# Kernel optimization log

Hardware: AMD Instinct MI355X
Metric: run time of the kernel (lower is better)

Reference implementation:

```python
import jax, jax.numpy as jnp
import numpy as np

T, B, H = 512, 256, 512


def setup_inputs() -> dict:
    key = jax.random.key(0)
    k1, k2, k3, k4, k5 = jax.random.split(key, 5)
    scale_i = 1.0 / np.sqrt(H)
    return {
        "h0": jax.random.normal(k1, (B, H), dtype=jnp.float32),
        "ins": jax.random.normal(k2, (T, B, H), dtype=jnp.float32),
        "Wi": jax.random.normal(k3, (H, 3 * H), dtype=jnp.float32) * scale_i,
        "bi": jnp.zeros((3 * H,), dtype=jnp.float32),
        "Wh": jax.random.normal(k4, (H, 3 * H), dtype=jnp.float32) * scale_i,
        "bhn": jnp.zeros((H,), dtype=jnp.float32),
        "resets": jax.random.randint(k5, (T, B), 0, 2).astype(jnp.bool_),
    }


def reference(h0, ins, Wi, bi, Wh, bhn, resets):
    # flax GRUCell math: r = sig(x Wir + bir + h Whr); z = sig(x Wiz + biz + h Whz)
    def step(h, xr):
        x, reset = xr                       # x: [B,H], reset: [B]
        h = jnp.where(reset[:, None], jnp.zeros_like(h), h)  # reset carry to zeros
        gi = x @ Wi + bi                    # [B,3H]
        gh = h @ Wh                         # [B,3H]
        ir, iz, inn = jnp.split(gi, 3, axis=-1)
        hr, hz, hn = jnp.split(gh, 3, axis=-1)
        r = jax.nn.sigmoid(ir + hr)
        z = jax.nn.sigmoid(iz + hz)
        n = jnp.tanh(inn + r * (hn + bhn))
        h_new = (1.0 - z) * n + z * h
        return h_new, h_new

    _, ys = jax.lax.scan(step, h0, (ins, resets))
    return ys                               # [T,B,H]
```

## Files before the change

kernel.cpp:

```cpp
#include <hip/hip_runtime.h>

#define T_ 512
#define B_ 256
#define H_ 512
#define NBINS 4112
typedef __bf16 bf16_t;
typedef __bf16 bf16x8 __attribute__((ext_vector_type(8)));
typedef float f32x4 __attribute__((ext_vector_type(4)));

__device__ __forceinline__ float bf2f(unsigned short u) {
  unsigned x = ((unsigned)u) << 16; float f; __builtin_memcpy(&f, &x, 4); return f;
}
__device__ __forceinline__ bf16x8 pack2(f32x4 a, f32x4 b) {
  bf16x8 w;
#pragma unroll
  for (int i = 0; i < 4; ++i) { w[i] = (bf16_t)a[i]; w[i + 4] = (bf16_t)b[i]; }
  return w;
}
__device__ __forceinline__ void st_sc1(float* p, float v) {
  asm volatile("global_store_dword %0, %1, off sc0 sc1" :: "v"(p), "v"(v) : "memory");
}
__device__ __forceinline__ void ld8_sc1(const float* p0, const float* p1,
                                        const float* p2, const float* p3,
                                        const float* p4, const float* p5,
                                        const float* p6, const float* p7,
                                        f32x4& v0, f32x4& v1, f32x4& v2, f32x4& v3,
                                        f32x4& v4, f32x4& v5, f32x4& v6, f32x4& v7) {
  asm volatile(
      "global_load_dwordx4 %0, %8, off sc0 sc1\n\t"
      "global_load_dwordx4 %1, %9, off sc0 sc1\n\t"
      "global_load_dwordx4 %2, %10, off sc0 sc1\n\t"
      "global_load_dwordx4 %3, %11, off sc0 sc1\n\t"
      "global_load_dwordx4 %4, %12, off sc0 sc1\n\t"
      "global_load_dwordx4 %5, %13, off sc0 sc1\n\t"
      "global_load_dwordx4 %6, %14, off sc0 sc1\n\t"
      "global_load_dwordx4 %7, %15, off sc0 sc1\n\t"
      "s_waitcnt vmcnt(0)"
      : "=&v"(v0), "=&v"(v1), "=&v"(v2), "=&v"(v3),
        "=&v"(v4), "=&v"(v5), "=&v"(v6), "=&v"(v7)
      : "v"(p0), "v"(p1), "v"(p2), "v"(p3), "v"(p4), "v"(p5), "v"(p6), "v"(p7)
      : "memory");
}
__device__ __forceinline__ float sigm(float x) { return 1.f / (1.f + __expf(-x)); }
__device__ __forceinline__ float tanh_(float a) { return 1.f - 2.f / (__expf(2.f * a) + 1.f); }

__global__ __launch_bounds__(64) void zero_meta(int* __restrict__ flags,
                                                int* __restrict__ bar) {
  int i = threadIdx.x;
  if (i < 4) flags[i] = 0;
  if (i < 8) bar[i] = 0;
}

__global__ __launch_bounds__(256) void detect_resets(const void* __restrict__ rst,
                                                     int n, int* __restrict__ flags) {
  const int* pi = (const int*)rst;
  const float* pf = (const float*)rst;
  int a = 0, bq = 0, c = 0;
  int nq = n >> 2;
  for (int i = blockIdx.x * 256 + threadIdx.x; i < nq; i += gridDim.x * 256) {
    int v = pi[i];
    if (v != 0 && v != 1) a = 1;
    float f = pf[i];
    if (!(f == 0.0f || f == 1.0f)) bq = 1;
    if ((i & 1) && v != 0) c = 1;
  }
  if (a) atomicOr(&flags[0], 1);
  if (bq) atomicOr(&flags[1], 1);
  if (c) atomicOr(&flags[2], 1);
}

__global__ __launch_bounds__(256) void convert_resets(const void* __restrict__ rst,
                                                      const int* __restrict__ flags,
                                                      unsigned char* __restrict__ r8,
                                                      int n) {
  const int* pi = (const int*)rst;
  const float* pf = (const float*)rst;
  int mode;
  if (flags[0] == 0) mode = flags[2] ? 0 : 3;
  else if (flags[1] == 0) mode = 1;
  else mode = 2;
  for (int i = blockIdx.x * 256 + threadIdx.x; i < n; i += gridDim.x * 256) {
    unsigned char v;
    if (mode == 0)      v = (unsigned char)(pi[i] != 0);
    else if (mode == 3) v = (unsigned char)(pi[2 * i] != 0);
    else if (mode == 1) v = (unsigned char)(pf[i] != 0.0f);
    else                v = ((const unsigned char*)rst)[i] ? 1 : 0;
    r8[i] = v;
  }
}

__global__ __launch_bounds__(256) void build_wc(const float* __restrict__ Wi,
                                                const float* __restrict__ Wh,
                                                bf16_t* __restrict__ Wc) {
  int id = blockIdx.x * 256 + threadIdx.x;
  int koct = id / 1536, n = id % 1536;
  const float* src = (koct < 64) ? Wi : Wh;
  int kk = (koct & 63) * 8;
  bf16x8 w;
#pragma unroll
  for (int e = 0; e < 8; ++e) w[e] = (bf16_t)src[(size_t)(kk + e) * 1536 + n];
  *(bf16x8*)(Wc + (size_t)id * 8) = w;
}

__device__ __forceinline__ int bucket_of(int t, int rs, int& p) {
  p = (t == 0 || rs) ? 0 : p + 1;
  return (p > 0) ? (p + 1) : ((t == 0 && !rs) ? 1 : 0);
}

__global__ __launch_bounds__(1024) void bins_kernel(const unsigned char* __restrict__ r8,
                                                    int* __restrict__ cur,
                                                    unsigned int* __restrict__ elem) {
  extern __shared__ int sm[];
  int* s0 = sm;
  int* s1 = sm + 8192;
  const int tid = threadIdx.x;
  for (int i = tid; i < 8192; i += 1024) s0[i] = 0;
  __syncthreads();
  if (tid < 256) {
    int b = tid, sub = b >> 5, p = 0;
    for (int t = 0; t < T_; ++t) {
      int bk = bucket_of(t, r8[t * B_ + b], p);
      atomicAdd(&s0[bk * 8 + sub], 1);
    }
  }
  __syncthreads();
  int* a = s0;
  int* bb = s1;
  for (int d = 1; d < 8192; d <<= 1) {
    for (int i = tid; i < 8192; i += 1024) bb[i] = a[i] + ((i >= d) ? a[i - d] : 0);
    __syncthreads();
    int* t = a; a = bb; bb = t;
  }
  for (int i = tid; i <= NBINS; i += 1024) cur[i] = (i == 0) ? 0 : a[i - 1];
  for (int i = tid; i < 8192; i += 1024)
    bb[i] = (i == 0) ? 0 : ((i <= NBINS) ? a[i - 1] : 0);
  __syncthreads();
  if (tid < 256) {
    int b = tid, sub = b >> 5, p = 0;
    for (int t = 0; t < T_; ++t) {
      int bk = bucket_of(t, r8[t * B_ + b], p);
      int pos = atomicAdd(&bb[bk * 8 + sub], 1);
      elem[pos] = (unsigned)(t * B_ + b);
    }
  }
}

template <int NRGC, int LDB>
__device__ __forceinline__ void mm3(const char* lds, const char* W, int q,
                                    int rgb, int span, int nrgd, int am, int aq,
                                    f32x4 (&acc)[3][NRGC]) {
  const char* Bp = W + (size_t)(q * 16 + am) * 16;
#pragma unroll
  for (int ks = 0; ks < 16; ++ks) {
    const int koct = ks * 4 + aq;
    const char* bb = Bp + (size_t)koct * 24576;
    bf16x8 b0 = *(const bf16x8*)(bb);
    bf16x8 b1 = *(const bf16x8*)(bb + 8192);
    bf16x8 b2 = *(const bf16x8*)(bb + 16384);
#pragma unroll
    for (int rg = 0; rg < NRGC; ++rg) {
      if (rg >= rgb && rg < rgb + span && rg < nrgd) {
        const int ar = rg * 16 + am;
        bf16x8 af = *(const bf16x8*)(lds + (size_t)ar * LDB +
                                     ((koct * 16) ^ ((ar & 7) << 4)));
        acc[0][rg] = __builtin_amdgcn_mfma_f32_16x16x32_bf16(af, b0, acc[0][rg], 0, 0, 0);
        acc[1][rg] = __builtin_amdgcn_mfma_f32_16x16x32_bf16(af, b1, acc[1][rg], 0, 0, 0);
        acc[2][rg] = __builtin_amdgcn_mfma_f32_16x16x32_bf16(af, b2, acc[2][rg], 0, 0, 0);
      }
    }
  }
}

template <int NKS, int NRGC, int LDB>
__device__ __forceinline__ void mm_block(const char* lds, const char* W, int q,
                                         int rgb, int span, int nrgd, int am, int aq,
                                         f32x4 (&acc)[4][NRGC]) {
  const char* Bp = W + (size_t)(q * 16 + am) * 16;
#pragma unroll
  for (int ks = 0; ks < NKS; ++ks) {
    const int koct = ks * 4 + aq;
    const char* bb = Bp + (size_t)koct * 24576;
    bf16x8 b0 = *(const bf16x8*)(bb);
    bf16x8 b1 = *(const bf16x8*)(bb + 8192);
    bf16x8 b2 = *(const bf16x8*)(bb + 16384);
#pragma unroll
    for (int rg = 0; rg < NRGC; ++rg) {
      if (rg >= rgb && rg < rgb + span && rg < nrgd) {
        const int ar = rg * 16 + am;
        bf16x8 af = *(const bf16x8*)(lds + (size_t)ar * LDB +
                                     ((koct * 16) ^ ((ar & 7) << 4)));
        acc[0][rg] = __builtin_amdgcn_mfma_f32_16x16x32_bf16(af, b0, acc[0][rg], 0, 0, 0);
        acc[1][rg] = __builtin_amdgcn_mfma_f32_16x16x32_bf16(af, b1, acc[1][rg], 0, 0, 0);
        if (ks < 16)
          acc[2][rg] = __builtin_amdgcn_mfma_f32_16x16x32_bf16(af, b2, acc[2][rg], 0, 0, 0);
        else
          acc[3][rg] = __builtin_amdgcn_mfma_f32_16x16x32_bf16(af, b2, acc[3][rg], 0, 0, 0);
      }
    }
  }
}

__global__ __launch_bounds__(512) void xonly_gemm(
    const float* __restrict__ ins, const bf16_t* __restrict__ Wic,
    const float* __restrict__ bi, const float* __restrict__ bhn,
    const unsigned char* __restrict__ r8, float* __restrict__ out) {
  extern __shared__ char lds[];
  const int u = blockIdx.x;
  const int tid = threadIdx.x, lane = tid & 63, w = tid >> 6;
  const int am = lane & 15, aq = lane >> 4;
  {
    const int tr = tid >> 2, tl = tid & 3;
    const float* xs = ins + ((size_t)u * 128 + tr) * 512;
    const int swz = (tr & 7) << 4;
    char* lrp = lds + tr * 1024;
#pragma unroll 4
    for (int s2 = 0; s2 < 16; ++s2) {
      const int ko = tl + 4 * s2;
      f32x4 a0 = __builtin_nontemporal_load((const f32x4*)(xs + ko * 8));
      f32x4 a1 = __builtin_nontemporal_load((const f32x4*)(xs + ko * 8 + 4));
      *(bf16x8*)(lrp + ((ko * 16) ^ swz)) = pack2(a0, a1);
    }
  }
  __syncthreads();
#pragma unroll 1
  for (int s = 0; s < 4; ++s) {
    const int q = w + 8 * s;
    f32x4 acc[3][8];
#pragma unroll
    for (int gg = 0; gg < 3; ++gg)
#pragma unroll
      for (int r = 0; r < 8; ++r) acc[gg][r] = (f32x4){0.f, 0.f, 0.f, 0.f};
    mm3<8, 1024>(lds, (const char*)Wic, q, 0, 8, 8, am, aq, acc);
    const int j = q * 16 + am;
    const float bir = bi[j], biz = bi[512 + j], bin = bi[1024 + j], bh = bhn[j];
#pragma unroll
    for (int rg = 0; rg < 8; ++rg) {
#pragma unroll
      for (int qq = 0; qq < 4; ++qq) {
        const int e = u * 128 + rg * 16 + aq * 4 + qq;
        if (r8[e]) {
          float r = sigm(acc[0][rg][qq] + bir);
          float z = sigm(acc[1][rg][qq] + biz);
          float n = tanh_(acc[2][rg][qq] + bin + r * bh);
          float v = (1.f - z) * n;
          float* op = out + (size_t)e * 512 + j;
          if (e >= (T_ - 1) * B_ || r8[e + B_]) __builtin_nontemporal_store(v, op);
          else st_sc1(op, v);
        }
      }
    }
  }
}

__global__ __launch_bounds__(512) void gru_pool(
    const float* __restrict__ ins, const float* __restrict__ h0,
    const bf16_t* __restrict__ Wc, const float* __restrict__ bi,
    const float* __restrict__ bhn, const unsigned char* __restrict__ r8,
    const unsigned int* __restrict__ elem, const int* __restrict__ cur,
    int* __restrict__ bar, float* __restrict__ out) {
  extern __shared__ char lds[];
  const int tid = threadIdx.x, lane = tid & 63, w = tid >> 6;
  const int am = lane & 15, aq = lane >> 4;
  const int nbg = gridDim.x, bg = blockIdx.x;
  int done = 0;

  for (int it = 1; it <= 513; ++it) {
    const int beg = cur[it * 8];
    const int cnt = cur[(it + 1) * 8] - beg;
    if (it >= 2 && cnt == 0) break;
    if (cnt > 0) {
      const int ntiles = (cnt + 63) >> 6;
      int lg = 0;
      while (lg < 4 && (ntiles << lg) < nbg) ++lg;
      const int nitems = ntiles << lg;
      const int Q = 32 >> lg;
      for (int i = bg; i < nitems; i += nbg) {
        const int u = i >> lg, jc = i & ((1 << lg) - 1);
        __syncthreads();
        {
          const int tr = tid >> 3, tl = tid & 7;
          const int row = u * 64 + tr;
          const float* xs = nullptr;
          const float* ph = nullptr;
          if (row < cnt) {
            const unsigned e = elem[beg + row];
            xs = ins + (size_t)e * 512;
            ph = (e < 256) ? (h0 + (size_t)e * 512) : (out + ((size_t)e - 256) * 512);
          }
          const int swz = (tr & 7) << 4;
          char* lrp = lds + tr * 2048;
#pragma unroll
          for (int s2 = 0; s2 < 8; ++s2) {
            const int ko = tl + 8 * s2;
            bf16x8 wv;
            if (xs) {
              f32x4 a0 = __builtin_nontemporal_load((const f32x4*)(xs + ko * 8));
              f32x4 a1 = __builtin_nontemporal_load((const f32x4*)(xs + ko * 8 + 4));
              wv = pack2(a0, a1);
            } else {
#pragma unroll
              for (int z = 0; z < 8; ++z) wv[z] = (bf16_t)0.f;
            }
            *(bf16x8*)(lrp + ((ko * 16) ^ swz)) = wv;
          }
          if (ph) {
#pragma unroll 1
            for (int hb = 0; hb < 2; ++hb) {
              f32x4 hv[8];
              const float* hp[8];
#pragma unroll
              for (int s2 = 0; s2 < 4; ++s2) {
                const int ko = tl + 8 * (8 + hb * 4 + s2);
                hp[2 * s2] = ph + (ko & 63) * 8;
                hp[2 * s2 + 1] = ph + (ko & 63) * 8 + 4;
              }
              ld8_sc1(hp[0], hp[1], hp[2], hp[3], hp[4], hp[5], hp[6], hp[7],
                      hv[0], hv[1], hv[2], hv[3], hv[4], hv[5], hv[6], hv[7]);
#pragma unroll
              for (int s2 = 0; s2 < 4; ++s2) {
                const int ko = tl + 8 * (8 + hb * 4 + s2);
                *(bf16x8*)(lrp + ((ko * 16) ^ swz)) = pack2(hv[2 * s2], hv[2 * s2 + 1]);
              }
            }
          } else {
#pragma unroll
            for (int s2 = 0; s2 < 8; ++s2) {
              const int ko = tl + 8 * (8 + s2);
              bf16x8 wv;
#pragma unroll
              for (int z = 0; z < 8; ++z) wv[z] = (bf16_t)0.f;
              *(bf16x8*)(lrp + ((ko * 16) ^ swz)) = wv;
            }
          }
        }
        __syncthreads();
        const int rem = cnt - u * 64;
        const int nrgd = ((rem < 64 ? rem : 64) + 15) >> 4;
        const int span = (Q >= 8) ? 4 : (Q >> 1);
        const int rgb = (Q >= 8) ? 0 : (w / Q) * span;
        const int nq = (Q >= 8) ? (Q >> 3) : 1;
#pragma unroll 1
    for (int s = 0; s < nq; ++s) {
          const int q = (Q >= 8) ? (jc * Q + w + 8 * s) : (jc * Q + (w & (Q - 1)));
          f32x4 acc[4][4];
#pragma unroll
          for (int gg = 0; gg < 4; ++gg)
#pragma unroll
            for (int r = 0; r < 4; ++r) acc[gg][r] = (f32x4){0.f, 0.f, 0.f, 0.f};
          mm_block<32, 4, 2048>(lds, (const char*)Wc, q, rgb, span, nrgd, am, aq, acc);
          const int j = q * 16 + am;
          const float bir = bi[j], biz = bi[512 + j], bin = bi[1024 + j], bh = bhn[j];
#pragma unroll
          for (int rg = 0; rg < 4; ++rg) {
            if (rg >= rgb && rg < rgb + span && rg < nrgd) {
#pragma unroll
              for (int qq = 0; qq < 4; ++qq) {
                const int lrow = rg * 16 + aq * 4 + qq;
                const int row = u * 64 + lrow;
                if (row < cnt) {
                  const unsigned e = elem[beg + row];
                  unsigned short hraw = *(const unsigned short*)(
                      lds + (size_t)lrow * 2048 +
                      (((64 + (j >> 3)) * 16) ^ ((lrow & 7) << 4)) + (j & 7) * 2);
                  float hp = bf2f(hraw);
                  float r = sigm(acc[0][rg][qq] + bir);
                  float z = sigm(acc[1][rg][qq] + biz);
                  float n = tanh_(acc[2][rg][qq] + bin + r * (acc[3][rg][qq] + bh));
                  float v = (1.f - z) * n + z * hp;
                  float* op = out + (size_t)e * 512 + j;
                  if (e >= (T_ - 1) * B_ || r8[e + B_]) *op = v;
                  else st_sc1(op, v);
                }
              }
            }
          }
        }
      }
    }
    __syncthreads();
    ++done;
    if (tid == 0) {
      __hip_atomic_fetch_add(&bar[0], 1, __ATOMIC_RELAXED, __HIP_MEMORY_SCOPE_AGENT);
      const int target = nbg * done;
      while (__hip_atomic_load(&bar[0], __ATOMIC_RELAXED, __HIP_MEMORY_SCOPE_AGENT) <
             target) {
        __builtin_amdgcn_s_sleep(2);
      }
    }
    __syncthreads();
  }
}

extern "C" void kernel_launch(void* const* d_in, const int* in_sizes, int n_in,
                              void* d_out, int out_size, void* d_ws, size_t ws_size,
                              hipStream_t stream) {
  const float* h0  = (const float*)d_in[0];
  const float* ins = (const float*)d_in[1];
  const float* Wi  = (const float*)d_in[2];
  const float* bi  = (const float*)d_in[3];
  const float* Wh  = (const float*)d_in[4];
  const float* bhn = (const float*)d_in[5];
  const void*  rst = d_in[6];
  float* out = (float*)d_out;

  char* ws = (char*)d_ws;
  const size_t off_r8    = 0;
  const size_t off_Wc    = 131072;
  const size_t off_flags = 3276800;
  const size_t off_bar   = 3276864;
  const size_t off_cur   = 3276928;
  const size_t off_elem  = 3293440;
  const size_t need      = 3817728;
  if (ws_size < need) return;

  unsigned char* r8 = (unsigned char*)(ws + off_r8);
  bf16_t* Wc = (bf16_t*)(ws + off_Wc);
  int* flags = (int*)(ws + off_flags);
  int* bar = (int*)(ws + off_bar);
  int* cur = (int*)(ws + off_cur);
  unsigned int* elem = (unsigned int*)(ws + off_elem);

  zero_meta<<<1, 64, 0, stream>>>(flags, bar);
  detect_resets<<<64, 256, 0, stream>>>(rst, T_ * B_, flags);
  convert_resets<<<128, 256, 0, stream>>>(rst, flags, r8, T_ * B_);
  build_wc<<<768, 256, 0, stream>>>(Wi, Wh, Wc);
  (void)hipFuncSetAttribute((const void*)bins_kernel,
                            hipFuncAttributeMaxDynamicSharedMemorySize, 65536);
  bins_kernel<<<1, 1024, 65536, stream>>>(r8, cur, elem);

  (void)hipFuncSetAttribute((const void*)xonly_gemm,
                            hipFuncAttributeMaxDynamicSharedMemorySize, 131072);
  xonly_gemm<<<1024, 512, 131072, stream>>>(ins, Wc, bi, bhn, r8, out);

  (void)hipFuncSetAttribute((const void*)gru_pool,
                            hipFuncAttributeMaxDynamicSharedMemorySize, 131072);
  void* args[] = {(void*)&ins, (void*)&h0, (void*)&Wc, (void*)&bi, (void*)&bhn,
                  (void*)&r8, (void*)&elem, (void*)&cur, (void*)&bar, (void*)&out};
  (void)hipLaunchCooperativeKernel((const void*)gru_pool, dim3(256), dim3(512),
                                   args, 131072, stream);
}
```

Before: 1.575 ms.

## Add 128-row tile path with cached bf16 inputs and flag-based grid barrier

The x-only GEMM now also writes bf16 copies of the inputs to a workspace buffer. The persistent GRU kernel uses them in a new 128-row tile path for large reset-bin levels, reading x fragments straight from global bf16 while only h is staged in LDS. The atomic-counter grid barrier becomes a per-block flag array that block 0 polls before writing a release flag. This aims to cut per-tile conversion and LDS traffic and lower barrier contention, at the cost of extra workspace, an extra write pass, and a path that needs enough workspace to run.

```diff
diff --git a/kernel.cpp b/kernel.cpp
--- a/kernel.cpp
+++ b/kernel.cpp
@@ -19,6 +19,15 @@
 }
 __device__ __forceinline__ void st_sc1(float* p, float v) {
   asm volatile("global_store_dword %0, %1, off sc0 sc1" :: "v"(p), "v"(v) : "memory");
+}
+__device__ __forceinline__ void st_flag(int* p, int v) {
+  asm volatile("global_store_dword %0, %1, off sc0 sc1" :: "v"(p), "v"(v) : "memory");
+}
+__device__ __forceinline__ int ld_flag(const int* p) {
+  int v;
+  asm volatile("global_load_dword %0, %1, off sc0 sc1\n\ts_waitcnt vmcnt(0)"
+               : "=v"(v) : "v"(p) : "memory");
+  return v;
 }
 __device__ __forceinline__ void ld8_sc1(const float* p0, const float* p1,
                                         const float* p2, const float* p3,
@@ -44,11 +53,13 @@
 __device__ __forceinline__ float sigm(float x) { return 1.f / (1.f + __expf(-x)); }
 __device__ __forceinline__ float tanh_(float a) { return 1.f - 2.f / (__expf(2.f * a) + 1.f); }
 
-__global__ __launch_bounds__(64) void zero_meta(int* __restrict__ flags,
-                                                int* __restrict__ bar) {
+__global__ __launch_bounds__(512) void zero_meta(int* __restrict__ flags,
+                                                 int* __restrict__ farr,
+                                                 int* __restrict__ rel) {
   int i = threadIdx.x;
   if (i < 4) flags[i] = 0;
-  if (i < 8) bar[i] = 0;
+  if (i < 256) farr[i] = 0;
+  if (i == 0) rel[0] = 0;
 }
 
 __global__ __launch_bounds__(256) void detect_resets(const void* __restrict__ rst,
@@ -200,17 +211,57 @@
   }
 }
 
+__device__ __forceinline__ void mm128(const char* lds, const bf16_t* const (&xp)[8],
+                                      const char* W, int q, int am, int aq,
+                                      f32x4 (&acc)[4][8]) {
+  const char* Bp = W + (size_t)(q * 16 + am) * 16;
+#pragma unroll 4
+  for (int ks = 0; ks < 16; ++ks) {
+    const int koct = ks * 4 + aq;
+    const char* bb = Bp + (size_t)koct * 24576;
+    bf16x8 b0 = *(const bf16x8*)(bb);
+    bf16x8 b1 = *(const bf16x8*)(bb + 8192);
+    bf16x8 b2 = *(const bf16x8*)(bb + 16384);
+#pragma unroll
+    for (int rg = 0; rg < 8; ++rg) {
+      bf16x8 af = *(const bf16x8*)(xp[rg] + koct * 8);
+      acc[0][rg] = __builtin_amdgcn_mfma_f32_16x16x32_bf16(af, b0, acc[0][rg], 0, 0, 0);
+      acc[1][rg] = __builtin_amdgcn_mfma_f32_16x16x32_bf16(af, b1, acc[1][rg], 0, 0, 0);
+      acc[2][rg] = __builtin_amdgcn_mfma_f32_16x16x32_bf16(af, b2, acc[2][rg], 0, 0, 0);
+    }
+  }
+#pragma unroll 4
+  for (int ks = 16; ks < 32; ++ks) {
+    const int koct = ks * 4 + aq;
+    const char* bb = Bp + (size_t)koct * 24576;
+    bf16x8 b0 = *(const bf16x8*)(bb);
+    bf16x8 b1 = *(const bf16x8*)(bb + 8192);
+    bf16x8 b2 = *(const bf16x8*)(bb + 16384);
+#pragma unroll
+    for (int rg = 0; rg < 8; ++rg) {
+      const int ar = rg * 16 + am;
+      bf16x8 af = *(const bf16x8*)(lds + (size_t)ar * 1024 +
+                                   (((koct - 64) * 16) ^ ((ar & 7) << 4)));
+      acc[0][rg] = __builtin_amdgcn_mfma_f32_16x16x32_bf16(af, b0, acc[0][rg], 0, 0, 0);
+      acc[1][rg] = __builtin_amdgcn_mfma_f32_16x16x32_bf16(af, b1, acc[1][rg], 0, 0, 0);
+      acc[3][rg] = __builtin_amdgcn_mfma_f32_16x16x32_bf16(af, b2, acc[3][rg], 0, 0, 0);
+    }
+  }
+}
+
 __global__ __launch_bounds__(512) void xonly_gemm(
     const float* __restrict__ ins, const bf16_t* __restrict__ Wic,
     const float* __restrict__ bi, const float* __restrict__ bhn,
-    const unsigned char* __restrict__ r8, float* __restrict__ out) {
+    const unsigned char* __restrict__ r8, bf16_t* __restrict__ xb,
+    float* __restrict__ out) {
   extern __shared__ char lds[];
   const int u = blockIdx.x;
   const int tid = threadIdx.x, lane = tid & 63, w = tid >> 6;
   const int am = lane & 15, aq = lane >> 4;
   {
     const int tr = tid >> 2, tl = tid & 3;
-    const float* xs = ins + ((size_t)u * 128 + tr) * 512;
+    const int row = u * 128 + tr;
+    const float* xs = ins + (size_t)row * 512;
     const int swz = (tr & 7) << 4;
     char* lrp = lds + tr * 1024;
 #pragma unroll 4
@@ -218,7 +269,9 @@
       const int ko = tl + 4 * s2;
       f32x4 a0 = __builtin_nontemporal_load((const f32x4*)(xs + ko * 8));
       f32x4 a1 = __builtin_nontemporal_load((const f32x4*)(xs + ko * 8 + 4));
-      *(bf16x8*)(lrp + ((ko * 16) ^ swz)) = pack2(a0, a1);
+      bf16x8 wv = pack2(a0, a1);
+      *(bf16x8*)(lrp + ((ko * 16) ^ swz)) = wv;
+      if (xb) __builtin_nontemporal_store(wv, (bf16x8*)(xb + (size_t)row * 512 + ko * 8));
     }
   }
   __syncthreads();
@@ -257,7 +310,8 @@
     const bf16_t* __restrict__ Wc, const float* __restrict__ bi,
     const float* __restrict__ bhn, const unsigned char* __restrict__ r8,
     const unsigned int* __restrict__ elem, const int* __restrict__ cur,
-    int* __restrict__ bar, float* __restrict__ out) {
+    const bf16_t* __restrict__ xb, int use128, int* __restrict__ farr,
+    int* __restrict__ rel, float* __restrict__ out) {
   extern __shared__ char lds[];
   const int tid = threadIdx.x, lane = tid & 63, w = tid >> 6;
   const int am = lane & 15, aq = lane >> 4;
@@ -268,7 +322,100 @@
     const int beg = cur[it * 8];
     const int cnt = cur[(it + 1) * 8] - beg;
     if (it >= 2 && cnt == 0) break;
-    if (cnt > 0) {
+    if (cnt >= 8192 && use128) {
+      const int ntiles = (cnt + 127) >> 7;
+      int lg = 0;
+      while (lg < 2 && (ntiles << lg) < nbg) ++lg;
+      const int nitems = ntiles << lg;
+      const int nsp = 4 >> lg;
+      for (int i = bg; i < nitems; i += nbg) {
+        const int u = i >> lg, sc = i & ((1 << lg) - 1);
+        __syncthreads();
+        {
+          const int tr = tid >> 2, tl = tid & 3;
+          const int row = u * 128 + tr;
+          const float* ph = nullptr;
+          if (row < cnt) {
+            const unsigned e = elem[beg + row];
+            ph = (e < 256) ? (h0 + (size_t)e * 512) : (out + ((size_t)e - 256) * 512);
+          }
+          const int swz = (tr & 7) << 4;
+          char* lrp = lds + tr * 1024;
+          if (ph) {
+#pragma unroll 1
+            for (int hb = 0; hb < 4; ++hb) {
+              f32x4 hv[8];
+              const float* hp[8];
+#pragma unroll
+              for (int s2 = 0; s2 < 4; ++s2) {
+                const int ko = tl * 16 + hb * 4 + s2;
+                hp[2 * s2] = ph + ko * 8;
+                hp[2 * s2 + 1] = ph + ko * 8 + 4;
+              }
+              ld8_sc1(hp[0], hp[1], hp[2], hp[3], hp[4], hp[5], hp[6], hp[7],
+                      hv[0], hv[1], hv[2], hv[3], hv[4], hv[5], hv[6], hv[7]);
+#pragma unroll
+              for (int s2 = 0; s2 < 4; ++s2) {
+                const int ko = tl * 16 + hb * 4 + s2;
+                *(bf16x8*)(lrp + ((ko * 16) ^ swz)) = pack2(hv[2 * s2], hv[2 * s2 + 1]);
+              }
+            }
+          } else {
+#pragma unroll
+            for (int s2 = 0; s2 < 16; ++s2) {
+              const int ko = tl * 16 + s2;
+              bf16x8 wv;
+#pragma unroll
+              for (int z = 0; z < 8; ++z) wv[z] = (bf16_t)0.f;
+              *(bf16x8*)(lrp + ((ko * 16) ^ swz)) = wv;
+            }
+          }
+        }
+        __syncthreads();
+        const bf16_t* xp[8];
+#pragma unroll
+        for (int rg = 0; rg < 8; ++rg) {
+          int row = u * 128 + rg * 16 + am;
+          int rc = (row < cnt) ? row : (cnt - 1);
+          xp[rg] = xb + (size_t)elem[beg + rc] * 512;
+        }
+#pragma unroll 1
+        for (int si = 0; si < nsp; ++si) {
+          const int s = sc * nsp + si;
+          const int q = w + 8 * s;
+          f32x4 acc[4][8];
+#pragma unroll
+          for (int gg = 0; gg < 4; ++gg)
+#pragma unroll
+            for (int r = 0; r < 8; ++r) acc[gg][r] = (f32x4){0.f, 0.f, 0.f, 0.f};
+          mm128(lds, xp, (const char*)Wc, q, am, aq, acc);
+          const int j = q * 16 + am;
+          const float bir = bi[j], biz = bi[512 + j], bin = bi[1024 + j], bh = bhn[j];
+#pragma unroll
+          for (int rg = 0; rg < 8; ++rg) {
+#pragma unroll
+            for (int qq = 0; qq < 4; ++qq) {
+              const int lrow = rg * 16 + aq * 4 + qq;
+              const int row = u * 128 + lrow;
+              if (row < cnt) {
+                const unsigned e = elem[beg + row];
+                unsigned short hraw = *(const unsigned short*)(
+                    lds + (size_t)lrow * 1024 +
+                    (((j >> 3) * 16) ^ ((lrow & 7) << 4)) + (j & 7) * 2);
+                float hp = bf2f(hraw);
+                float r = sigm(acc[0][rg][qq] + bir);
+                float z = sigm(acc[1][rg][qq] + biz);
+                float n = tanh_(acc[2][rg][qq] + bin + r * (acc[3][rg][qq] + bh));
+                float v = (1.f - z) * n + z * hp;
+                float* op = out + (size_t)e * 512 + j;
+                if (e >= (T_ - 1) * B_ || r8[e + B_]) *op = v;
+                else st_sc1(op, v);
+              }
+            }
+          }
+        }
+      }
+    } else if (cnt > 0) {
       const int ntiles = (cnt + 63) >> 6;
       int lg = 0;
       while (lg < 4 && (ntiles << lg) < nbg) ++lg;
@@ -340,7 +487,7 @@
         const int rgb = (Q >= 8) ? 0 : (w / Q) * span;
         const int nq = (Q >= 8) ? (Q >> 3) : 1;
 #pragma unroll 1
-    for (int s = 0; s < nq; ++s) {
+        for (int s = 0; s < nq; ++s) {
           const int q = (Q >= 8) ? (jc * Q + w + 8 * s) : (jc * Q + (w & (Q - 1)));
           f32x4 acc[4][4];
 #pragma unroll
@@ -379,13 +526,17 @@
     }
     __syncthreads();
     ++done;
+    if (tid == 0) st_flag(&farr[bg], done);
+    if (bg == 0) {
+      for (;;) {
+        int f = (tid < nbg) ? ld_flag(&farr[tid]) : done;
+        if (__syncthreads_count(f >= done) == (int)blockDim.x) break;
+        __builtin_amdgcn_s_sleep(1);
+      }
+      if (tid == 0) st_flag(rel, done);
+    }
     if (tid == 0) {
-      __hip_atomic_fetch_add(&bar[0], 1, __ATOMIC_RELAXED, __HIP_MEMORY_SCOPE_AGENT);
-      const int target = nbg * done;
-      while (__hip_atomic_load(&bar[0], __ATOMIC_RELAXED, __HIP_MEMORY_SCOPE_AGENT) <
-             target) {
-        __builtin_amdgcn_s_sleep(2);
-      }
+      while (ld_flag(rel) < done) __builtin_amdgcn_s_sleep(1);
     }
     __syncthreads();
   }
@@ -407,20 +558,26 @@
   const size_t off_r8    = 0;
   const size_t off_Wc    = 131072;
   const size_t off_flags = 3276800;
-  const size_t off_bar   = 3276864;
-  const size_t off_cur   = 3276928;
-  const size_t off_elem  = 3293440;
-  const size_t need      = 3817728;
+  const size_t off_farr  = 3276864;
+  const size_t off_rel   = 3277888;
+  const size_t off_cur   = 3277952;
+  const size_t off_elem  = 3294464;
+  const size_t off_xb    = 3818752;
+  const size_t need      = 3818752;
+  const size_t need_xb   = off_xb + (size_t)131072 * 512 * 2;
   if (ws_size < need) return;
+  const int use128 = (ws_size >= need_xb) ? 1 : 0;
 
   unsigned char* r8 = (unsigned char*)(ws + off_r8);
   bf16_t* Wc = (bf16_t*)(ws + off_Wc);
   int* flags = (int*)(ws + off_flags);
-  int* bar = (int*)(ws + off_bar);
+  int* farr = (int*)(ws + off_farr);
+  int* rel = (int*)(ws + off_rel);
   int* cur = (int*)(ws + off_cur);
   unsigned int* elem = (unsigned int*)(ws + off_elem);
-
-  zero_meta<<<1, 64, 0, stream>>>(flags, bar);
+  bf16_t* xb = use128 ? (bf16_t*)(ws + off_xb) : nullptr;
+
+  zero_meta<<<1, 512, 0, stream>>>(flags, farr, rel);
   detect_resets<<<64, 256, 0, stream>>>(rst, T_ * B_, flags);
   convert_resets<<<128, 256, 0, stream>>>(rst, flags, r8, T_ * B_);
   build_wc<<<768, 256, 0, stream>>>(Wi, Wh, Wc);
@@ -430,12 +587,13 @@
 
   (void)hipFuncSetAttribute((const void*)xonly_gemm,
                             hipFuncAttributeMaxDynamicSharedMemorySize, 131072);
-  xonly_gemm<<<1024, 512, 131072, stream>>>(ins, Wc, bi, bhn, r8, out);
+  xonly_gemm<<<1024, 512, 131072, stream>>>(ins, Wc, bi, bhn, r8, xb, out);
 
   (void)hipFuncSetAttribute((const void*)gru_pool,
                             hipFuncAttributeMaxDynamicSharedMemorySize, 131072);
   void* args[] = {(void*)&ins, (void*)&h0, (void*)&Wc, (void*)&bi, (void*)&bhn,
-                  (void*)&r8, (void*)&elem, (void*)&cur, (void*)&bar, (void*)&out};
+                  (void*)&r8, (void*)&elem, (void*)&cur, (void*)&xb,
+                  (void*)&use128, (void*)&farr, (void*)&rel, (void*)&out};
   (void)hipLaunchCooperativeKernel((const void*)gru_pool, dim3(256), dim3(512),
                                    args, 131072, stream);
 }
```

After: 2.013 ms. 1.28x slower.

## Replace atomic grid barrier with flag-array gather/release and transpose reset bits

Applied to the files above, without the earlier changes.

Replaces the grid-wide barrier in the persistent GRU kernel. Before, every block did an atomic add on one counter and spun on it. Now each block writes its own flag slot, block 0 polls all flags with a block-wide count, and then publishes a release word that the other blocks spin on. This is meant to cut atomic contention and polling traffic on a single cache line at every step. Separately, the reset mask is also stored transposed so the binning kernel can read four timesteps per word with coalesced loads. This adds an extra byte buffer and a two-hop barrier latency through block 0.

```diff
diff --git a/kernel.cpp b/kernel.cpp
--- a/kernel.cpp
+++ b/kernel.cpp
@@ -19,6 +19,15 @@
 }
 __device__ __forceinline__ void st_sc1(float* p, float v) {
   asm volatile("global_store_dword %0, %1, off sc0 sc1" :: "v"(p), "v"(v) : "memory");
+}
+__device__ __forceinline__ void st_flag(int* p, int v) {
+  asm volatile("global_store_dword %0, %1, off sc0 sc1" :: "v"(p), "v"(v) : "memory");
+}
+__device__ __forceinline__ int ld_flag(const int* p) {
+  int v;
+  asm volatile("global_load_dword %0, %1, off sc0 sc1\n\ts_waitcnt vmcnt(0)"
+               : "=v"(v) : "v"(p) : "memory");
+  return v;
 }
 __device__ __forceinline__ void ld8_sc1(const float* p0, const float* p1,
                                         const float* p2, const float* p3,
@@ -44,11 +53,13 @@
 __device__ __forceinline__ float sigm(float x) { return 1.f / (1.f + __expf(-x)); }
 __device__ __forceinline__ float tanh_(float a) { return 1.f - 2.f / (__expf(2.f * a) + 1.f); }
 
-__global__ __launch_bounds__(64) void zero_meta(int* __restrict__ flags,
-                                                int* __restrict__ bar) {
+__global__ __launch_bounds__(512) void zero_meta(int* __restrict__ flags,
+                                                 int* __restrict__ farr,
+                                                 int* __restrict__ rel) {
   int i = threadIdx.x;
   if (i < 4) flags[i] = 0;
-  if (i < 8) bar[i] = 0;
+  if (i < 256) farr[i] = 0;
+  if (i == 0) rel[0] = 0;
 }
 
 __global__ __launch_bounds__(256) void detect_resets(const void* __restrict__ rst,
@@ -72,6 +83,7 @@
 __global__ __launch_bounds__(256) void convert_resets(const void* __restrict__ rst,
                                                       const int* __restrict__ flags,
                                                       unsigned char* __restrict__ r8,
+                                                      unsigned char* __restrict__ r8t,
                                                       int n) {
   const int* pi = (const int*)rst;
   const float* pf = (const float*)rst;
@@ -86,6 +98,7 @@
     else if (mode == 1) v = (unsigned char)(pf[i] != 0.0f);
     else                v = ((const unsigned char*)rst)[i] ? 1 : 0;
     r8[i] = v;
+    r8t[(i & 255) * 512 + (i >> 8)] = v;
   }
 }
 
@@ -107,7 +120,7 @@
   return (p > 0) ? (p + 1) : ((t == 0 && !rs) ? 1 : 0);
 }
 
-__global__ __launch_bounds__(1024) void bins_kernel(const unsigned char* __restrict__ r8,
+__global__ __launch_bounds__(1024) void bins_kernel(const unsigned char* __restrict__ r8t,
                                                     int* __restrict__ cur,
                                                     unsigned int* __restrict__ elem) {
   extern __shared__ int sm[];
@@ -118,9 +131,15 @@
   __syncthreads();
   if (tid < 256) {
     int b = tid, sub = b >> 5, p = 0;
-    for (int t = 0; t < T_; ++t) {
-      int bk = bucket_of(t, r8[t * B_ + b], p);
-      atomicAdd(&s0[bk * 8 + sub], 1);
+    const unsigned* rp = (const unsigned*)(r8t + b * 512);
+#pragma unroll 4
+    for (int tw = 0; tw < 128; ++tw) {
+      unsigned v = rp[tw];
+#pragma unroll
+      for (int e = 0; e < 4; ++e) {
+        int bk = bucket_of(tw * 4 + e, (v >> (8 * e)) & 255, p);
+        atomicAdd(&s0[bk * 8 + sub], 1);
+      }
     }
   }
   __syncthreads();
@@ -137,10 +156,17 @@
   __syncthreads();
   if (tid < 256) {
     int b = tid, sub = b >> 5, p = 0;
-    for (int t = 0; t < T_; ++t) {
-      int bk = bucket_of(t, r8[t * B_ + b], p);
-      int pos = atomicAdd(&bb[bk * 8 + sub], 1);
-      elem[pos] = (unsigned)(t * B_ + b);
+    const unsigned* rp = (const unsigned*)(r8t + b * 512);
+#pragma unroll 4
+    for (int tw = 0; tw < 128; ++tw) {
+      unsigned v = rp[tw];
+#pragma unroll
+      for (int e = 0; e < 4; ++e) {
+        int t = tw * 4 + e;
+        int bk = bucket_of(t, (v >> (8 * e)) & 255, p);
+        int pos = atomicAdd(&bb[bk * 8 + sub], 1);
+        elem[pos] = (unsigned)(t * B_ + b);
+      }
     }
   }
 }
@@ -257,7 +283,7 @@
     const bf16_t* __restrict__ Wc, const float* __restrict__ bi,
     const float* __restrict__ bhn, const unsigned char* __restrict__ r8,
     const unsigned int* __restrict__ elem, const int* __restrict__ cur,
-    int* __restrict__ bar, float* __restrict__ out) {
+    int* __restrict__ farr, int* __restrict__ rel, float* __restrict__ out) {
   extern __shared__ char lds[];
   const int tid = threadIdx.x, lane = tid & 63, w = tid >> 6;
   const int am = lane & 15, aq = lane >> 4;
@@ -340,7 +366,7 @@
         const int rgb = (Q >= 8) ? 0 : (w / Q) * span;
         const int nq = (Q >= 8) ? (Q >> 3) : 1;
 #pragma unroll 1
-    for (int s = 0; s < nq; ++s) {
+        for (int s = 0; s < nq; ++s) {
           const int q = (Q >= 8) ? (jc * Q + w + 8 * s) : (jc * Q + (w & (Q - 1)));
           f32x4 acc[4][4];
 #pragma unroll
@@ -379,13 +405,17 @@
     }
     __syncthreads();
     ++done;
+    if (tid == 0) st_flag(&farr[bg], done);
+    if (bg == 0) {
+      for (;;) {
+        int f = (tid < nbg) ? ld_flag(&farr[tid]) : done;
+        if (__syncthreads_count(f >= done) == (int)blockDim.x) break;
+        __builtin_amdgcn_s_sleep(1);
+      }
+      if (tid == 0) st_flag(rel, done);
+    }
     if (tid == 0) {
-      __hip_atomic_fetch_add(&bar[0], 1, __ATOMIC_RELAXED, __HIP_MEMORY_SCOPE_AGENT);
-      const int target = nbg * done;
-      while (__hip_atomic_load(&bar[0], __ATOMIC_RELAXED, __HIP_MEMORY_SCOPE_AGENT) <
-             target) {
-        __builtin_amdgcn_s_sleep(2);
-      }
+      while (ld_flag(rel) < done) __builtin_amdgcn_s_sleep(1);
     }
     __syncthreads();
   }
@@ -405,28 +435,32 @@
 
   char* ws = (char*)d_ws;
   const size_t off_r8    = 0;
-  const size_t off_Wc    = 131072;
-  const size_t off_flags = 3276800;
-  const size_t off_bar   = 3276864;
-  const size_t off_cur   = 3276928;
-  const size_t off_elem  = 3293440;
-  const size_t need      = 3817728;
+  const size_t off_r8t   = 131072;
+  const size_t off_Wc    = 262144;
+  const size_t off_flags = 3407872;
+  const size_t off_farr  = 3407936;
+  const size_t off_rel   = 3408960;
+  const size_t off_cur   = 3409024;
+  const size_t off_elem  = 3425536;
+  const size_t need      = 3949824;
   if (ws_size < need) return;
 
   unsigned char* r8 = (unsigned char*)(ws + off_r8);
+  unsigned char* r8t = (unsigned char*)(ws + off_r8t);
   bf16_t* Wc = (bf16_t*)(ws + off_Wc);
   int* flags = (int*)(ws + off_flags);
-  int* bar = (int*)(ws + off_bar);
+  int* farr = (int*)(ws + off_farr);
+  int* rel = (int*)(ws + off_rel);
   int* cur = (int*)(ws + off_cur);
   unsigned int* elem = (unsigned int*)(ws + off_elem);
 
-  zero_meta<<<1, 64, 0, stream>>>(flags, bar);
+  zero_meta<<<1, 512, 0, stream>>>(flags, farr, rel);
   detect_resets<<<64, 256, 0, stream>>>(rst, T_ * B_, flags);
-  convert_resets<<<128, 256, 0, stream>>>(rst, flags, r8, T_ * B_);
+  convert_resets<<<128, 256, 0, stream>>>(rst, flags, r8, r8t, T_ * B_);
   build_wc<<<768, 256, 0, stream>>>(Wi, Wh, Wc);
   (void)hipFuncSetAttribute((const void*)bins_kernel,
                             hipFuncAttributeMaxDynamicSharedMemorySize, 65536);
-  bins_kernel<<<1, 1024, 65536, stream>>>(r8, cur, elem);
+  bins_kernel<<<1, 1024, 65536, stream>>>(r8t, cur, elem);
 
   (void)hipFuncSetAttribute((const void*)xonly_gemm,
                             hipFuncAttributeMaxDynamicSharedMemorySize, 131072);
@@ -435,7 +469,8 @@
   (void)hipFuncSetAttribute((const void*)gru_pool,
                             hipFuncAttributeMaxDynamicSharedMemorySize, 131072);
   void* args[] = {(void*)&ins, (void*)&h0, (void*)&Wc, (void*)&bi, (void*)&bhn,
-                  (void*)&r8, (void*)&elem, (void*)&cur, (void*)&bar, (void*)&out};
+                  (void*)&r8, (void*)&elem, (void*)&cur, (void*)&farr,
+                  (void*)&rel, (void*)&out};
   (void)hipLaunchCooperativeKernel((const void*)gru_pool, dim3(256), dim3(512),
                                    args, 131072, stream);
 }
```

After: 1.458 ms. 1.08x faster.
